# Optimization experiments

Hardware: AMD Instinct MI355X
Metric: run time of the kernel (lower is better)

## Reference

```python
import jax, jax.numpy as jnp
import numpy as np

T = 32768   # time points
N = 256     # state dim
NI = 32     # input dim
NO = 32     # output dim

# Dopri5 Butcher tableau (solution weights; b7 = 0 so only 6 stages needed)
_C = np.array([0.0, 1/5, 3/10, 4/5, 8/9, 1.0], dtype=np.float32)
_A21 = 1/5
_A31, _A32 = 3/40, 9/40
_A41, _A42, _A43 = 44/45, -56/15, 32/9
_A51, _A52, _A53, _A54 = 19372/6561, -25360/2187, 64448/6561, -212/729
_A61, _A62, _A63, _A64, _A65 = 9017/3168, -355/33, 46732/5247, 49/176, -5103/18656
_B1, _B3, _B4, _B5, _B6 = 35/384, 500/1113, 125/192, -2187/6784, 11/84

# Hermite cubic basis evaluated at the 6 stage offsets c in [0,1]: H[s, j]
s = _C
_H = np.stack([2*s**3 - 3*s**2 + 1,   # h00 * u_n
               s**3 - 2*s**2 + s,     # h10 * m_n (dt-scaled slope)
               -2*s**3 + 3*s**2,      # h01 * u_{n+1}
               s**3 - s**2], axis=1).astype(np.float32)  # h11 * m_{n+1}


def setup_inputs() -> dict:
    key = jax.random.key(0)
    k1, k2, k3, k4, k5, k6 = jax.random.split(key, 6)
    t = jnp.arange(T, dtype=jnp.float32)  # uniform grid, dt = 1
    u = jax.random.normal(k1, (T, NI), jnp.float32)
    x0 = jax.random.normal(k2, (N,), jnp.float32)
    # Stable linear system so fixed-step integration does not blow up
    A = jax.random.normal(k3, (N, N), jnp.float32) * (0.01 / np.sqrt(N)) - 0.02 * jnp.eye(N, dtype=jnp.float32)
    B = jax.random.normal(k4, (N, NI), jnp.float32) * (0.01 / np.sqrt(NI))
    C = jax.random.normal(k5, (NO, N), jnp.float32) / np.sqrt(N)
    D = jax.random.normal(k6, (NO, NI), jnp.float32) / np.sqrt(NI)
    return {"t": t, "u": u, "initial_state": x0, "A": A, "B": B, "C": C, "D": D}


def _stage_inputs(u):
    """Cubic-Hermite interpolation of u at the 6 Dopri5 stage times of each interval.
    Slopes via finite differences (dt-scaled, so index units suffice on a uniform grid).
    Returns [T-1, 6, NI]."""
    m = jnp.concatenate([u[1:2] - u[0:1],
                         (u[2:] - u[:-2]) * 0.5,
                         u[-1:] - u[-2:-1]], axis=0)
    P = jnp.stack([u[:-1], m[:-1], u[1:], m[1:]], axis=1)  # [T-1, 4, NI]
    return jnp.einsum('sj,tjd->tsd', jnp.asarray(_H), P)


def reference(t, u, initial_state, A, B, C, D):
    dt = t[1] - t[0]
    us = _stage_inputs(u)  # [T-1, 6, NI]

    def f(x, uu):  # vector field: dx/dt = A x + B u(t)
        return A @ x + B @ uu

    def step(x, us_n):
        k1 = f(x, us_n[0])
        k2 = f(x + dt * (_A21 * k1), us_n[1])
        k3 = f(x + dt * (_A31 * k1 + _A32 * k2), us_n[2])
        k4 = f(x + dt * (_A41 * k1 + _A42 * k2 + _A43 * k3), us_n[3])
        k5 = f(x + dt * (_A51 * k1 + _A52 * k2 + _A53 * k3 + _A54 * k4), us_n[4])
        k6 = f(x + dt * (_A61 * k1 + _A62 * k2 + _A63 * k3 + _A64 * k4 + _A65 * k5), us_n[5])
        x_new = x + dt * (_B1 * k1 + _B3 * k3 + _B4 * k4 + _B5 * k5 + _B6 * k6)
        return x_new, x_new

    _, xs = jax.lax.scan(step, initial_state, us)
    x = jnp.concatenate([initial_state[None], xs], axis=0)  # [T, N]
    y = x @ C.T + u @ D.T  # output: y = C x + D u, vmapped over time by broadcasting
    return (x, y)
```

## Files before the change

kernel.cpp:

```cpp
#include <hip/hip_runtime.h>


#define TPTS 32768

typedef __attribute__((ext_vector_type(8))) short short8;
typedef __attribute__((ext_vector_type(4))) float float4v;
typedef unsigned short ushort_t;

__device__ __forceinline__ ushort_t bf16_hi(float f) {
  unsigned u = __builtin_bit_cast(unsigned, f);
  unsigned r = (u + 0x7FFFu + ((u >> 16) & 1u)) >> 16;
  return (ushort_t)r;
}
__device__ __forceinline__ float bf16_f(ushort_t h) {
  unsigned u = ((unsigned)h) << 16;
  return __builtin_bit_cast(float, u);
}

template <int MODE, int CLEN>
__global__ __launch_bounds__(1024, 4) void chain_mfma(const ushort_t* Mh, const ushort_t* Ml,
                                                      const float* X0, const float* V,
                                                      float* Out, ushort_t* OutH, ushort_t* OutL) {
  constexpr int STEPS = (MODE == 0) ? CLEN : CLEN - 1;
  constexpr int HSLOTS = (MODE == 2) ? 5 : 1;
  int blk = blockIdx.x, t = threadIdx.x;
  int w = t >> 6, l = t & 63;
  int q = l >> 4, c16 = l & 15;
  int n0 = w * 16;
  short8 bh[8], bl[8];
#pragma unroll
  for (int kt = 0; kt < 8; kt++) {
    size_t offs = (size_t)(n0 + c16) * 256 + kt * 32 + q * 8;
    bh[kt] = *(const short8*)(Mh + offs);
    bl[kt] = *(const short8*)(Ml + offs);
  }
  __shared__ __attribute__((aligned(16))) ushort_t xh[2][32][16][8];
  __shared__ __attribute__((aligned(16))) ushort_t xl[2][32][16][8];
  __shared__ float hist[HSLOTS][16][256];
  {
    int e = t;
    int c = e >> 6, qq = (e & 63) * 4;
    int cg = blk * 16 + c;
    float4 v4;
    if (MODE == 0) {
      v4 = make_float4(qq == cg ? 1.f : 0.f, qq + 1 == cg ? 1.f : 0.f,
                       qq + 2 == cg ? 1.f : 0.f, qq + 3 == cg ? 1.f : 0.f);
    } else if (MODE == 1) {
      v4 = *(const float4*)(V + (size_t)cg * CLEN * 256 + qq);
    } else {
      v4 = *(const float4*)(X0 + (size_t)cg * 256 + qq);
      *(float4*)(Out + ((size_t)cg * CLEN) * 256 + qq) = v4;
    }
    float vals[4] = {v4.x, v4.y, v4.z, v4.w};
#pragma unroll
    for (int i = 0; i < 4; i++) {
      int n = qq + i;
      ushort_t h = bf16_hi(vals[i]);
      xh[0][n >> 3][c][n & 7] = h;
      xl[0][n >> 3][c][n & 7] = bf16_hi(vals[i] - bf16_f(h));
    }
  }
  float vnext[4];
  if (MODE != 0) {
#pragma unroll
    for (int r = 0; r < 4; r++) {
      int cg = blk * 16 + q * 4 + r;
      int drow = (MODE == 1) ? 1 : 0;
      vnext[r] = V[((size_t)cg * CLEN + drow) * 256 + n0 + c16];
    }
  }
  __syncthreads();
// ... 1 lines not shown
    int cur = (s - 1) & 1, nxt = s & 1;
    if (MODE == 2 && s >= 5 && ((s - 1) & 3) == 0) {
      int rbase = s - 4;
      for (int e = t; e < 4096; e += 1024) {
        int slot = e >> 10;
        int rem = e & 1023;
        int c = rem >> 6, qq = (rem & 63) * 4;
        int row = rbase + slot;
        int cg = blk * 16 + c;
        *(float4*)(Out + ((size_t)cg * CLEN + row) * 256 + qq) = *(const float4*)&hist[row % 5][c][qq];
      }
    }
    float vc[4];
    if (MODE != 0) {
#pragma unroll
      for (int i2 = 0; i2 < 4; i2++) vc[i2] = vnext[i2];
      if (s < STEPS) {
        int drow = (MODE == 1) ? (s + 1) : s;
#pragma unroll
        for (int r = 0; r < 4; r++)
          vnext[r] = V[((size_t)(blk * 16 + q * 4 + r) * CLEN + drow) * 256 + n0 + c16];
      }
    }
#pragma unroll
    for (int kt = 0; kt < 8; kt++) {
      asm volatile("" : "+v"(bh[kt]));
      asm volatile("" : "+v"(bl[kt]));
    }
    float4v aH = {0.f, 0.f, 0.f, 0.f};
    float4v aL = {0.f, 0.f, 0.f, 0.f};
    float4v aC = {0.f, 0.f, 0.f, 0.f};
#pragma unroll
    for (int kt = 0; kt < 8; kt++) {
      short8 ah = *(const short8*)&xh[cur][kt * 4 + q][c16][0];
      short8 al = *(const short8*)&xl[cur][kt * 4 + q][c16][0];
      aH = __builtin_amdgcn_mfma_f32_16x16x32_bf16(ah, bh[kt], aH, 0, 0, 0);
      aL = __builtin_amdgcn_mfma_f32_16x16x32_bf16(al, bh[kt], aL, 0, 0, 0);
      aC = __builtin_amdgcn_mfma_f32_16x16x32_bf16(ah, bl[kt], aC, 0, 0, 0);
    }
#pragma unroll
    for (int r = 0; r < 4; r++) {
      int c = q * 4 + r;
      int n = n0 + c16;
      float val = aH[r] + aL[r] + aC[r];
      if (MODE != 0) val += vc[r];
      int cg = blk * 16 + c;
      if (MODE == 2) hist[s % 5][c][n] = val;
      if (MODE == 1 && s == STEPS) Out[(size_t)cg * 256 + n] = val;
      if (MODE == 0 && s == STEPS) {
        ushort_t h2 = bf16_hi(val);
        Out[(size_t)n * 256 + cg] = val;
        OutH[(size_t)n * 256 + cg] = h2;
        OutL[(size_t)n * 256 + cg] = bf16_hi(val - bf16_f(h2));
      }
      ushort_t h = bf16_hi(val);
      xh[nxt][n >> 3][c][n & 7] = h;
      xl[nxt][n >> 3][c][n & 7] = bf16_hi(val - bf16_f(h));
    }
    __syncthreads();
  }
  if (MODE == 2) {
    for (int e = t; e < 3072; e += 1024) {
      int slot = e >> 10;
      int rem = e & 1023;
      int c = rem >> 6, qq = (rem & 63) * 4;
      int row = (STEPS - 2) + slot;
      int cg = blk * 16 + c;
      *(float4*)(Out + ((size_t)cg * CLEN + row) * 256 + qq) = *(const float4*)&hist[row % 5][c][qq];
    }
  }
}

__global__ __launch_bounds__(256) void gemm128(const float* __restrict__ A, const float* __restrict__ B,
                                               float* __restrict__ C, int M, int K) {
  int m0 = blockIdx.x * 128, n0 = blockIdx.y * 128;
  __shared__ float As[8][128];
  __shared__ float Bs[8][128];
  int tid = threadIdx.x;
  int am = tid >> 1, akc = (tid & 1) * 4;
  int bk = tid >> 5, bn = (tid & 31) * 4;
  int ty = tid >> 4, tx = tid & 15;
  float acc[8][8] = {{0.f}};
  for (int kt = 0; kt < K; kt += 8) {
    float4 av = make_float4(0.f, 0.f, 0.f, 0.f);
    if (m0 + am < M) av = *(const float4*)(A + (size_t)(m0 + am) * K + kt + akc);
    float4 bv = *(const float4*)(B + (size_t)(kt + bk) * 256 + n0 + bn);
    __syncthreads();
    As[akc + 0][am] = av.x;
    As[akc + 1][am] = av.y;
    As[akc + 2][am] = av.z;
    As[akc + 3][am] = av.w;
    *(float4*)&Bs[bk][bn] = bv;
    __syncthreads();
#pragma unroll
    for (int kk = 0; kk < 8; kk++) {
      float4 a0 = *(const float4*)&As[kk][ty * 8];
      float4 a1 = *(const float4*)&As[kk][ty * 8 + 4];
      float4 b0 = *(const float4*)&Bs[kk][tx * 8];
      float4 b1 = *(const float4*)&Bs[kk][tx * 8 + 4];
      float ar[8] = {a0.x, a0.y, a0.z, a0.w, a1.x, a1.y, a1.z, a1.w};
      float br[8] = {b0.x, b0.y, b0.z, b0.w, b1.x, b1.y, b1.z, b1.w};
#pragma unroll
      for (int i = 0; i < 8; i++)
#pragma unroll
        for (int j = 0; j < 8; j++) acc[i][j] += ar[i] * br[j];
    }
  }
#pragma unroll
  for (int i = 0; i < 8; i++) {
    int row = m0 + ty * 8 + i;
    if (row < M) {
      *(float4*)&C[(size_t)row * 256 + n0 + tx * 8] = make_float4(acc[i][0], acc[i][1], acc[i][2], acc[i][3]);
      *(float4*)&C[(size_t)row * 256 + n0 + tx * 8 + 4] = make_float4(acc[i][4], acc[i][5], acc[i][6], acc[i][7]);
    }
  }
}

__global__ __launch_bounds__(256) void transpose_at(const float* __restrict__ A, float* __restrict__ AT) {
  __shared__ float tile[64][65];
  int bx = blockIdx.x & 3, by = blockIdx.x >> 2;
  int r0 = by * 64, c0 = bx * 64;
  int t = threadIdx.x;
  int lr = t >> 4, lc = (t & 15) * 4;
  for (int rr = lr; rr < 64; rr += 16) {
    float4 v = *(const float4*)(A + (size_t)(r0 + rr) * 256 + c0 + lc);
    tile[rr][lc + 0] = v.x; tile[rr][lc + 1] = v.y; tile[rr][lc + 2] = v.z; tile[rr][lc + 3] = v.w;
  }
  __syncthreads();
  for (int rr = lr; rr < 64; rr += 16) {
    float4 v = make_float4(tile[lc + 0][rr], tile[lc + 1][rr], tile[lc + 2][rr], tile[lc + 3][rr]);
    *(float4*)(AT + (size_t)(c0 + rr) * 256 + r0 + lc) = v;
  }
}

__global__ __launch_bounds__(1024) void unit_resp(const float* __restrict__ AT,
                                                  const float* __restrict__ Bm,
                                                  float* __restrict__ Rout,
                                                  ushort_t* __restrict__ Rh,
                                                  ushort_t* __restrict__ Rl,
                                                  float* __restrict__ FcatT) {
  int blk = blockIdx.x;
  int tid = threadIdx.x;
  int jg = tid >> 8;
  int i = tid & 255;
  int cc = jg;
  int col = blk * 4 + cc;

  __shared__ float xs4[256][4];
  __shared__ float4 part[4][256];

  const float AA[6][5] = {
      {0.f, 0.f, 0.f, 0.f, 0.f},
      {0.2f, 0.f, 0.f, 0.f, 0.f},
      {3.f / 40.f, 9.f / 40.f, 0.f, 0.f, 0.f},
      {44.f / 45.f, -56.f / 15.f, 32.f / 9.f, 0.f, 0.f},
// ... 45 lines not shown
    float acx = 0.f, acy = 0.f, acz = 0.f, acw = 0.f;
#pragma unroll 8
    for (int jj = 0; jj < 64; jj++) {
      int j = j0 + jj;
      float a = AT[(size_t)j * 256 + i];
      float4 xv = *(const float4*)xs4[j];
      acx += a * xv.x;
      acy += a * xv.y;
      acz += a * xv.z;
      acw += a * xv.w;
    }
    part[jg][i] = make_float4(acx, acy, acz, acw);
    __syncthreads();
    float k = bh[s];
#pragma unroll
    for (int g = 0; g < 4; g++) {
      const float* p = (const float*)&part[g][i];
      k += p[cc];
    }
    kreg[s] = k;
  }

  float o = xc;
#pragma unroll
  for (int s = 0; s < 6; s++) o += BB[s] * kreg[s];
  if (!isF) {
    Rout[(size_t)i * 256 + col] = o;
    ushort_t h = bf16_hi(o);
    Rh[(size_t)i * 256 + col] = h;
    Rl[(size_t)i * 256 + col] = bf16_hi(o - bf16_f(h));
  } else {
    FcatT[(size_t)(col - 256) * 256 + i] = o;
  }
}

__global__ __launch_bounds__(128) void build_wtap(const float* __restrict__ u, float* __restrict__ Wtap) {
  int n = blockIdx.x;
  int tid = threadIdx.x;
  int t = tid >> 5, c = tid & 31;
  float val = 0.f;
  if (n < TPTS - 1) {
    if (t == 0) val = u[(size_t)n * 32 + c];
    else if (t == 2) val = u[(size_t)(n + 1) * 32 + c];
    else {
      int k = (t == 1) ? n : n + 1;
      if (k == 0) val = u[32 + c] - u[c];
      else if (k == TPTS - 1) val = u[(size_t)(TPTS - 1) * 32 + c] - u[(size_t)(TPTS - 2) * 32 + c];
      else val = 0.5f * (u[(size_t)(k + 1) * 32 + c] - u[(size_t)(k - 1) * 32 + c]);
    }
  }
  Wtap[(size_t)n * 128 + tid] = val;
}

__global__ __launch_bounds__(256) void top_scan(const float* __restrict__ V3, const float* __restrict__ x0,
                                                const float* __restrict__ R512, float* __restrict__ X3) {
  int k = blockIdx.x, i = threadIdx.x;
  if (k == 0) { X3[i] = x0[i]; return; }
  __shared__ float va[256];
  __shared__ float inner[256];
  if (k == 1) {
    inner[i] = x0[i];
  } else {
    const float* vecA = (k == 2) ? x0 : (V3 + (size_t)(k - 3) * 256);
    va[i] = vecA[i];
    __syncthreads();
    float acc = V3[(size_t)(k - 2) * 256 + i];
    const float* rr = R512 + (size_t)i * 256;
    for (int j = 0; j < 256; j += 4) {
      float4 rv = *(const float4*)(rr + j);
      acc += rv.x * va[j] + rv.y * va[j + 1] + rv.z * va[j + 2] + rv.w * va[j + 3];
    }
    inner[i] = acc;
  }
  __syncthreads();
  float acc2 = V3[(size_t)(k - 1) * 256 + i];
  const float* rr2 = R512 + (size_t)i * 256;
  for (int j = 0; j < 256; j += 4) {
    float4 rv = *(const float4*)(rr2 + j);
    acc2 += rv.x * inner[j] + rv.y * inner[j + 1] + rv.z * inner[j + 2] + rv.w * inner[j + 3];
  }
  X3[(size_t)k * 256 + i] = acc2;
}

__global__ __launch_bounds__(256) void y_kernel(const float* __restrict__ x, const float* __restrict__ u,
                                                const float* __restrict__ Cm, const float* __restrict__ Dm,
                                                float* __restrict__ y) {
  __shared__ float CsT[256][36];
  __shared__ float DsT[32][36];
  int tid = threadIdx.x;
  for (int k = tid; k < 8192; k += 256) CsT[k & 255][k >> 8] = Cm[k];
  for (int k = tid; k < 1024; k += 256) DsT[k & 31][k >> 5] = Dm[k];
  __syncthreads();
  int rt = tid >> 3, ct = tid & 7;
  int n0 = blockIdx.x * 128 + rt * 4;
  int o0 = ct * 4;
  float acc[4][4] = {{0.f}};
#pragma unroll 4
  for (int i = 0; i < 256; i += 4) {
    float4 cv0 = *(const float4*)&CsT[i + 0][o0];
    float4 cv1 = *(const float4*)&CsT[i + 1][o0];
    float4 cv2 = *(const float4*)&CsT[i + 2][o0];
    float4 cv3 = *(const float4*)&CsT[i + 3][o0];
#pragma unroll
    for (int r = 0; r < 4; r++) {
      float4 xv = *(const float4*)(x + (size_t)(n0 + r) * 256 + i);
      acc[r][0] += xv.x * cv0.x + xv.y * cv1.x + xv.z * cv2.x + xv.w * cv3.x;
      acc[r][1] += xv.x * cv0.y + xv.y * cv1.y + xv.z * cv2.y + xv.w * cv3.y;
      acc[r][2] += xv.x * cv0.z + xv.y * cv1.z + xv.z * cv2.z + xv.w * cv3.z;
      acc[r][3] += xv.x * cv0.w + xv.y * cv1.w + xv.z * cv2.w + xv.w * cv3.w;
    }
  }
#pragma unroll
  for (int i = 0; i < 32; i += 4) {
    float4 dv0 = *(const float4*)&DsT[i + 0][o0];
    float4 dv1 = *(const float4*)&DsT[i + 1][o0];
    float4 dv2 = *(const float4*)&DsT[i + 2][o0];
    float4 dv3 = *(const float4*)&DsT[i + 3][o0];
#pragma unroll
    for (int r = 0; r < 4; r++) {
      float4 uv = *(const float4*)(u + (size_t)(n0 + r) * 32 + i);
      acc[r][0] += uv.x * dv0.x + uv.y * dv1.x + uv.z * dv2.x + uv.w * dv3.x;
      acc[r][1] += uv.x * dv0.y + uv.y * dv1.y + uv.z * dv2.y + uv.w * dv3.y;
      acc[r][2] += uv.x * dv0.z + uv.y * dv1.z + uv.z * dv2.z + uv.w * dv3.z;
      acc[r][3] += uv.x * dv0.w + uv.y * dv1.w + uv.z * dv2.w + uv.w * dv3.w;
    }
  }
#pragma unroll
  for (int r = 0; r < 4; r++)
    *(float4*)(y + (size_t)(n0 + r) * 32 + o0) =
        make_float4(acc[r][0], acc[r][1], acc[r][2], acc[r][3]);
}

extern "C" void kernel_launch(void* const* d_in, const int* in_sizes, int n_in,
                              void* d_out, int out_size, void* d_ws, size_t ws_size,
                              hipStream_t stream) {
  const float* u  = (const float*)d_in[1];
  const float* x0 = (const float*)d_in[2];
  const float* A  = (const float*)d_in[3];
  const float* Bm = (const float*)d_in[4];
  const float* Cm = (const float*)d_in[5];
  const float* Dm = (const float*)d_in[6];
  float* xout = (float*)d_out;
  float* yout = xout + (size_t)TPTS * 256;

  char* wsb = (char*)d_ws;
  size_t off = 0;
  auto alloc = [&](size_t bytes) -> void* {
    void* p = (void*)(wsb + off);
    off = (off + bytes + 255) & ~(size_t)255;
    return p;
  };
  float*    Rfp    = (float*)alloc(65536 * 4);
  ushort_t* Rh     = (ushort_t*)alloc(65536 * 2);
  ushort_t* Rl     = (ushort_t*)alloc(65536 * 2);
  float*    PowFp  = (float*)alloc(65536 * 4);
  ushort_t* R8h    = (ushort_t*)alloc(65536 * 2);
  ushort_t* R8l    = (ushort_t*)alloc(65536 * 2);
  ushort_t* R64h   = (ushort_t*)alloc(65536 * 2);
  ushort_t* R64l   = (ushort_t*)alloc(65536 * 2);
  float*    R512fp = (float*)alloc(65536 * 4);
  ushort_t* R512h  = (ushort_t*)alloc(65536 * 2);
  ushort_t* R512l  = (ushort_t*)alloc(65536 * 2);
  float*    ATm    = (float*)alloc(65536 * 4);
  float*    FcatT  = (float*)alloc(128 * 256 * 4);
  float*    Wtap   = (float*)alloc((size_t)TPTS * 128 * 4);
  float*    V0     = (float*)alloc((size_t)TPTS * 256 * 4);
  float*    V1     = (float*)alloc(4096 * 256 * 4);
  float*    V2     = (float*)alloc(512 * 256 * 4);
  float*    V3     = (float*)alloc(64 * 256 * 4);
  float*    X3     = (float*)alloc(64 * 256 * 4);
  float*    X2     = (float*)alloc(512 * 256 * 4);
  float*    X1     = (float*)alloc(4096 * 256 * 4);
  (void)ws_size; (void)in_sizes; (void)n_in; (void)out_size;

  transpose_at<<<dim3(16), dim3(256), 0, stream>>>(A, ATm);
  unit_resp<<<dim3(96), dim3(1024), 0, stream>>>(ATm, Bm, Rfp, Rh, Rl, FcatT);

  chain_mfma<0, 8><<<dim3(16), dim3(1024), 0, stream>>>(Rh, Rl, nullptr, nullptr, PowFp, R8h, R8l);
  chain_mfma<0, 8><<<dim3(16), dim3(1024), 0, stream>>>(R8h, R8l, nullptr, nullptr, PowFp, R64h, R64l);
  chain_mfma<0, 8><<<dim3(16), dim3(1024), 0, stream>>>(R64h, R64l, nullptr, nullptr, R512fp, R512h, R512l);

  build_wtap<<<dim3(TPTS), dim3(128), 0, stream>>>(u, Wtap);
  gemm128<<<dim3(256, 2), dim3(256), 0, stream>>>(Wtap, FcatT, V0, TPTS, 128);

  chain_mfma<1, 8><<<dim3(256), dim3(1024), 0, stream>>>(Rh, Rl, nullptr, V0, V1, nullptr, nullptr);
  chain_mfma<1, 8><<<dim3(32), dim3(1024), 0, stream>>>(R8h, R8l, nullptr, V1, V2, nullptr, nullptr);
  chain_mfma<1, 8><<<dim3(4), dim3(1024), 0, stream>>>(R64h, R64l, nullptr, V2, V3, nullptr, nullptr);

  top_scan<<<dim3(64), dim3(256), 0, stream>>>(V3, x0, R512fp, X3);
  chain_mfma<2, 8><<<dim3(4), dim3(1024), 0, stream>>>(R64h, R64l, X3, V2, X2, nullptr, nullptr);
  chain_mfma<2, 8><<<dim3(32), dim3(1024), 0, stream>>>(R8h, R8l, X2, V1, X1, nullptr, nullptr);
  chain_mfma<2, 8><<<dim3(256), dim3(1024), 0, stream>>>(Rh, Rl, X1, V0, xout, nullptr, nullptr);

  y_kernel<<<dim3(256), dim3(256), 0, stream>>>(xout, u, Cm, Dm, yout);
}
```

Before: 342.3 us.

## Fuse scan chain into persistent megakernel with grid barriers and fused drive GEMM

Replaces about ten separate chain, top-scan and output kernel launches with one persistent 256-block kernel. The stages are separated by a software grid barrier built on atomics, and independent stages (power chains and the first-level scan) share phases. The Wtap build is folded into the GEMM's operand load, which removes a large intermediate buffer and one launch. The design relies on all 256 blocks of 1024 threads being co-resident, since the barrier would deadlock otherwise, and it adds barrier latency while many blocks sit idle in the small phases.

Result: slower. 1.111 ms (+224.5%).

```diff
diff --git a/kernel.cpp b/kernel.cpp
--- a/kernel.cpp
+++ b/kernel.cpp
@@ -17,16 +17,36 @@
   return __builtin_bit_cast(float, u);
 }
 
+__device__ __forceinline__ void grid_bar(unsigned* cnt, unsigned* gen) {
+  __syncthreads();
+  if (threadIdx.x == 0) {
+    __threadfence();
+    unsigned g = __hip_atomic_load(gen, __ATOMIC_RELAXED, __HIP_MEMORY_SCOPE_AGENT);
+    unsigned a = __hip_atomic_fetch_add(cnt, 1u, __ATOMIC_ACQ_REL, __HIP_MEMORY_SCOPE_AGENT);
+    if (a == 255u) {
+      __hip_atomic_store(cnt, 0u, __ATOMIC_RELAXED, __HIP_MEMORY_SCOPE_AGENT);
+      __hip_atomic_store(gen, g + 1u, __ATOMIC_RELEASE, __HIP_MEMORY_SCOPE_AGENT);
+    } else {
+      while (__hip_atomic_load(gen, __ATOMIC_ACQUIRE, __HIP_MEMORY_SCOPE_AGENT) == g)
+        __builtin_amdgcn_s_sleep(2);
+    }
+    __threadfence();
+  }
+  __syncthreads();
+}
+
 template <int MODE, int CLEN>
-__global__ __launch_bounds__(1024, 4) void chain_mfma(const ushort_t* Mh, const ushort_t* Ml,
-                                                      const float* X0, const float* V,
-                                                      float* Out, ushort_t* OutH, ushort_t* OutL) {
+__device__ __forceinline__ void chain_body(char* arena, const ushort_t* Mh, const ushort_t* Ml,
+                                           const float* X0, const float* V,
+                                           float* Out, ushort_t* OutH, ushort_t* OutL, int blk) {
   constexpr int STEPS = (MODE == 0) ? CLEN : CLEN - 1;
-  constexpr int HSLOTS = (MODE == 2) ? 5 : 1;
-  int blk = blockIdx.x, t = threadIdx.x;
+  int t = threadIdx.x;
   int w = t >> 6, l = t & 63;
   int q = l >> 4, c16 = l & 15;
   int n0 = w * 16;
+  ushort_t (*xh)[32][16][8] = reinterpret_cast<ushort_t(*)[32][16][8]>(arena);
+  ushort_t (*xl)[32][16][8] = reinterpret_cast<ushort_t(*)[32][16][8]>(arena + 16384);
+  float (*hist)[16][256] = reinterpret_cast<float(*)[16][256]>(arena + 32768);
   short8 bh[8], bl[8];
 #pragma unroll
   for (int kt = 0; kt < 8; kt++) {
@@ -34,9 +54,6 @@
     bh[kt] = *(const short8*)(Mh + offs);
     bl[kt] = *(const short8*)(Ml + offs);
   }
-  __shared__ __attribute__((aligned(16))) ushort_t xh[2][32][16][8];
-  __shared__ __attribute__((aligned(16))) ushort_t xl[2][32][16][8];
-  __shared__ float hist[HSLOTS][16][256];
   {
     int e = t;
     int c = e >> 6, qq = (e & 63) * 4;
@@ -104,11 +121,13 @@
     float4v aC = {0.f, 0.f, 0.f, 0.f};
 #pragma unroll
     for (int kt = 0; kt < 8; kt++) {
-      short8 ah = *(const short8*)&xh[cur][kt * 4 + q][c16][0];
-      short8 al = *(const short8*)&xl[cur][kt * 4 + q][c16][0];
-      aH = __builtin_amdgcn_mfma_f32_16x16x32_bf16(ah, bh[kt], aH, 0, 0, 0);
-      aL = __builtin_amdgcn_mfma_f32_16x16x32_bf16(al, bh[kt], aL, 0, 0, 0);
-      aC = __builtin_amdgcn_mfma_f32_16x16x32_bf16(ah, bl[kt], aC, 0, 0, 0);
+      short8 ah = *(const short8*)&(*xh)[0][0][0];
+      (void)ah;
+      short8 ah2 = *(const short8*)&xh[cur][kt * 4 + q][c16][0];
+      short8 al2 = *(const short8*)&xl[cur][kt * 4 + q][c16][0];
+      aH = __builtin_amdgcn_mfma_f32_16x16x32_bf16(ah2, bh[kt], aH, 0, 0, 0);
+      aL = __builtin_amdgcn_mfma_f32_16x16x32_bf16(al2, bh[kt], aL, 0, 0, 0);
+      aC = __builtin_amdgcn_mfma_f32_16x16x32_bf16(ah2, bl[kt], aC, 0, 0, 0);
     }
 #pragma unroll
     for (int r = 0; r < 4; r++) {
@@ -143,8 +162,148 @@
   }
 }
 
-__global__ __launch_bounds__(256) void gemm128(const float* __restrict__ A, const float* __restrict__ B,
-                                               float* __restrict__ C, int M, int K) {
+__global__ __launch_bounds__(1024, 4) void mega_scan(
+    const ushort_t* Rh, const ushort_t* Rl,
+    ushort_t* R8h, ushort_t* R8l, ushort_t* R64h, ushort_t* R64l,
+    float* R512fp, ushort_t* R512h, ushort_t* R512l, float* PowFp,
+    const float* V0, float* V1, float* V2, float* V3,
+    const float* x0, float* X3, float* X2, float* X1,
+    float* xout, const float* u, const float* Cm, const float* Dm, float* yout,
+    unsigned* bar) {
+  __shared__ __attribute__((aligned(16))) char arena[114688];
+  int blk = blockIdx.x;
+  int t = threadIdx.x;
+  unsigned* cnt = bar;
+  unsigned* gen = bar + 1;
+
+  if (blk < 16)
+    chain_body<0, 8>(arena, Rh, Rl, nullptr, nullptr, PowFp, R8h, R8l, blk);
+  else
+    chain_body<1, 8>(arena, Rh, Rl, nullptr, V0, V1, nullptr, nullptr, blk - 16);
+  grid_bar(cnt, gen);
+
+  if (blk < 16)
+    chain_body<1, 8>(arena, Rh, Rl, nullptr, V0, V1, nullptr, nullptr, 240 + blk);
+  else if (blk < 32)
+    chain_body<0, 8>(arena, R8h, R8l, nullptr, nullptr, PowFp, R64h, R64l, blk - 16);
+  grid_bar(cnt, gen);
+
+  if (blk < 32)
+    chain_body<1, 8>(arena, R8h, R8l, nullptr, V1, V2, nullptr, nullptr, blk);
+  else if (blk < 48)
+    chain_body<0, 8>(arena, R64h, R64l, nullptr, nullptr, R512fp, R512h, R512l, blk - 32);
+  grid_bar(cnt, gen);
+
+  if (blk < 4)
+    chain_body<1, 8>(arena, R64h, R64l, nullptr, V2, V3, nullptr, nullptr, blk);
+  grid_bar(cnt, gen);
+
+  {
+    float* va = ((float*)arena) + (t >> 8) * 256;
+    float* inner = ((float*)arena) + 1024 + (t >> 8) * 256;
+    int ug = t >> 8, i = t & 255;
+    int k = blk * 4 + ug;
+    bool act = (blk < 16);
+    if (act) {
+      if (k >= 3)      va[i] = V3[(size_t)(k - 3) * 256 + i];
+      else if (k == 2) va[i] = x0[i];
+      else             va[i] = 0.f;
+    }
+    __syncthreads();
+    if (act) {
+      float innv = 0.f;
+      if (k == 1) innv = x0[i];
+      else if (k >= 2) {
+        float acc = V3[(size_t)(k - 2) * 256 + i];
+        const float* rr = R512fp + (size_t)i * 256;
+        for (int j = 0; j < 256; j += 4) {
+          float4 rv = *(const float4*)(rr + j);
+          acc += rv.x * va[j] + rv.y * va[j + 1] + rv.z * va[j + 2] + rv.w * va[j + 3];
+        }
+        innv = acc;
+      }
+      inner[i] = innv;
+    }
+    __syncthreads();
+    if (act) {
+      if (k == 0) {
+        X3[i] = x0[i];
+      } else {
+        float acc2 = V3[(size_t)(k - 1) * 256 + i];
+        const float* rr2 = R512fp + (size_t)i * 256;
+        for (int j = 0; j < 256; j += 4) {
+          float4 rv = *(const float4*)(rr2 + j);
+          acc2 += rv.x * inner[j] + rv.y * inner[j + 1] + rv.z * inner[j + 2] + rv.w * inner[j + 3];
+        }
+        X3[(size_t)k * 256 + i] = acc2;
+      }
+    }
+  }
+  grid_bar(cnt, gen);
+
+  if (blk < 4)
+    chain_body<2, 8>(arena, R64h, R64l, X3, V2, X2, nullptr, nullptr, blk);
+  grid_bar(cnt, gen);
+
+  if (blk < 32)
+    chain_body<2, 8>(arena, R8h, R8l, X2, V1, X1, nullptr, nullptr, blk);
+  grid_bar(cnt, gen);
+
+  chain_body<2, 8>(arena, Rh, Rl, X1, V0, xout, nullptr, nullptr, blk);
+  grid_bar(cnt, gen);
+
+  {
+    float (*CsT)[36] = reinterpret_cast<float(*)[36]>(arena);
+    float (*DsT)[36] = reinterpret_cast<float(*)[36]>(arena + 36864);
+    for (int k2 = t; k2 < 8192; k2 += 1024) CsT[k2 & 255][k2 >> 8] = Cm[k2];
+    for (int k2 = t; k2 < 1024; k2 += 1024) DsT[k2 & 31][k2 >> 5] = Dm[k2];
+    __syncthreads();
+    if (t < 256) {
+      int rt = t >> 3, ct = t & 7;
+      int n0 = blk * 128 + rt * 4;
+      int o0 = ct * 4;
+      float acc[4][4] = {{0.f}};
+#pragma unroll 4
+      for (int i = 0; i < 256; i += 4) {
+        float4 cv0 = *(const float4*)&CsT[i + 0][o0];
+        float4 cv1 = *(const float4*)&CsT[i + 1][o0];
+        float4 cv2 = *(const float4*)&CsT[i + 2][o0];
+        float4 cv3 = *(const float4*)&CsT[i + 3][o0];
+#pragma unroll
+        for (int r = 0; r < 4; r++) {
+          float4 xv = *(const float4*)(xout + (size_t)(n0 + r) * 256 + i);
+          acc[r][0] += xv.x * cv0.x + xv.y * cv1.x + xv.z * cv2.x + xv.w * cv3.x;
+          acc[r][1] += xv.x * cv0.y + xv.y * cv1.y + xv.z * cv2.y + xv.w * cv3.y;
+          acc[r][2] += xv.x * cv0.z + xv.y * cv1.z + xv.z * cv2.z + xv.w * cv3.z;
+          acc[r][3] += xv.x * cv0.w + xv.y * cv1.w + xv.z * cv2.w + xv.w * cv3.w;
+        }
+      }
+#pragma unroll
+      for (int i = 0; i < 32; i += 4) {
+        float4 dv0 = *(const float4*)&DsT[i + 0][o0];
+        float4 dv1 = *(const float4*)&DsT[i + 1][o0];
+        float4 dv2 = *(const float4*)&DsT[i + 2][o0];
+        float4 dv3 = *(const float4*)&DsT[i + 3][o0];
+#pragma unroll
+        for (int r = 0; r < 4; r++) {
+          float4 uv = *(const float4*)(u + (size_t)(n0 + r) * 32 + i);
+          acc[r][0] += uv.x * dv0.x + uv.y * dv1.x + uv.z * dv2.x + uv.w * dv3.x;
+          acc[r][1] += uv.x * dv0.y + uv.y * dv1.y + uv.z * dv2.y + uv.w * dv3.y;
+          acc[r][2] += uv.x * dv0.z + uv.y * dv1.z + uv.z * dv2.z + uv.w * dv3.z;
+          acc[r][3] += uv.x * dv0.w + uv.y * dv1.w + uv.z * dv2.w + uv.w * dv3.w;
+        }
+      }
+#pragma unroll
+      for (int r = 0; r < 4; r++)
+        *(float4*)(yout + (size_t)(n0 + r) * 32 + o0) =
+            make_float4(acc[r][0], acc[r][1], acc[r][2], acc[r][3]);
+    }
+  }
+}
+
+__global__ __launch_bounds__(256) void gemm_drive(const float* __restrict__ u,
+                                                  const float* __restrict__ B,
+                                                  float* __restrict__ C, int M) {
   int m0 = blockIdx.x * 128, n0 = blockIdx.y * 128;
   __shared__ float As[8][128];
   __shared__ float Bs[8][128];
@@ -152,10 +311,41 @@
   int am = tid >> 1, akc = (tid & 1) * 4;
   int bk = tid >> 5, bn = (tid & 31) * 4;
   int ty = tid >> 4, tx = tid & 15;
+  int n = m0 + am;
   float acc[8][8] = {{0.f}};
-  for (int kt = 0; kt < K; kt += 8) {
+  for (int kt = 0; kt < 128; kt += 8) {
+    int tt = kt >> 5;
+    int cb = (kt & 31) + akc;
     float4 av = make_float4(0.f, 0.f, 0.f, 0.f);
-    if (m0 + am < M) av = *(const float4*)(A + (size_t)(m0 + am) * K + kt + akc);
+    if (n < TPTS - 1) {
+      if (tt == 0) {
+        av = *(const float4*)(u + (size_t)n * 32 + cb);
+      } else if (tt == 1) {
+        if (n == 0) {
+          float4 a1 = *(const float4*)(u + 32 + cb);
+          float4 a0 = *(const float4*)(u + cb);
+          av = make_float4(a1.x - a0.x, a1.y - a0.y, a1.z - a0.z, a1.w - a0.w);
+        } else {
+          float4 ap = *(const float4*)(u + (size_t)(n + 1) * 32 + cb);
+          float4 am4 = *(const float4*)(u + (size_t)(n - 1) * 32 + cb);
+          av = make_float4(0.5f * (ap.x - am4.x), 0.5f * (ap.y - am4.y),
+                           0.5f * (ap.z - am4.z), 0.5f * (ap.w - am4.w));
+        }
+      } else if (tt == 2) {
+        av = *(const float4*)(u + (size_t)(n + 1) * 32 + cb);
+      } else {
+        if (n + 1 == TPTS - 1) {
+          float4 a1 = *(const float4*)(u + (size_t)(TPTS - 1) * 32 + cb);
+          float4 a0 = *(const float4*)(u + (size_t)(TPTS - 2) * 32 + cb);
+          av = make_float4(a1.x - a0.x, a1.y - a0.y, a1.z - a0.z, a1.w - a0.w);
+        } else {
+          float4 ap = *(const float4*)(u + (size_t)(n + 2) * 32 + cb);
+          float4 am4 = *(const float4*)(u + (size_t)n * 32 + cb);
+          av = make_float4(0.5f * (ap.x - am4.x), 0.5f * (ap.y - am4.y),
+                           0.5f * (ap.z - am4.z), 0.5f * (ap.w - am4.w));
+        }
+      }
+    }
     float4 bv = *(const float4*)(B + (size_t)(kt + bk) * 256 + n0 + bn);
     __syncthreads();
     As[akc + 0][am] = av.x;
@@ -188,11 +378,13 @@
   }
 }
 
-__global__ __launch_bounds__(256) void transpose_at(const float* __restrict__ A, float* __restrict__ AT) {
+__global__ __launch_bounds__(256) void transpose_at(const float* __restrict__ A, float* __restrict__ AT,
+                                                    unsigned* bar) {
   __shared__ float tile[64][65];
   int bx = blockIdx.x & 3, by = blockIdx.x >> 2;
   int r0 = by * 64, c0 = bx * 64;
   int t = threadIdx.x;
+  if (blockIdx.x == 0 && t == 0) { bar[0] = 0u; bar[1] = 0u; }
   int lr = t >> 4, lc = (t & 15) * 4;
   for (int rr = lr; rr < 64; rr += 16) {
     float4 v = *(const float4*)(A + (size_t)(r0 + rr) * 256 + c0 + lc);
@@ -304,103 +496,6 @@
   } else {
     FcatT[(size_t)(col - 256) * 256 + i] = o;
   }
-}
-
-__global__ __launch_bounds__(128) void build_wtap(const float* __restrict__ u, float* __restrict__ Wtap) {
-  int n = blockIdx.x;
-  int tid = threadIdx.x;
-  int t = tid >> 5, c = tid & 31;
-  float val = 0.f;
-  if (n < TPTS - 1) {
-    if (t == 0) val = u[(size_t)n * 32 + c];
-    else if (t == 2) val = u[(size_t)(n + 1) * 32 + c];
-    else {
-      int k = (t == 1) ? n : n + 1;
-      if (k == 0) val = u[32 + c] - u[c];
-      else if (k == TPTS - 1) val = u[(size_t)(TPTS - 1) * 32 + c] - u[(size_t)(TPTS - 2) * 32 + c];
-      else val = 0.5f * (u[(size_t)(k + 1) * 32 + c] - u[(size_t)(k - 1) * 32 + c]);
-    }
-  }
-  Wtap[(size_t)n * 128 + tid] = val;
-}
-
-__global__ __launch_bounds__(256) void top_scan(const float* __restrict__ V3, const float* __restrict__ x0,
-                                                const float* __restrict__ R512, float* __restrict__ X3) {
-  int k = blockIdx.x, i = threadIdx.x;
-  if (k == 0) { X3[i] = x0[i]; return; }
-  __shared__ float va[256];
-  __shared__ float inner[256];
-  if (k == 1) {
-    inner[i] = x0[i];
-  } else {
-    const float* vecA = (k == 2) ? x0 : (V3 + (size_t)(k - 3) * 256);
-    va[i] = vecA[i];
-    __syncthreads();
-    float acc = V3[(size_t)(k - 2) * 256 + i];
-    const float* rr = R512 + (size_t)i * 256;
-    for (int j = 0; j < 256; j += 4) {
-      float4 rv = *(const float4*)(rr + j);
-      acc += rv.x * va[j] + rv.y * va[j + 1] + rv.z * va[j + 2] + rv.w * va[j + 3];
-    }
-    inner[i] = acc;
-  }
-  __syncthreads();
-  float acc2 = V3[(size_t)(k - 1) * 256 + i];
-  const float* rr2 = R512 + (size_t)i * 256;
-  for (int j = 0; j < 256; j += 4) {
-    float4 rv = *(const float4*)(rr2 + j);
-    acc2 += rv.x * inner[j] + rv.y * inner[j + 1] + rv.z * inner[j + 2] + rv.w * inner[j + 3];
-  }
-  X3[(size_t)k * 256 + i] = acc2;
-}
-
-__global__ __launch_bounds__(256) void y_kernel(const float* __restrict__ x, const float* __restrict__ u,
-                                                const float* __restrict__ Cm, const float* __restrict__ Dm,
-                                                float* __restrict__ y) {
-  __shared__ float CsT[256][36];
-  __shared__ float DsT[32][36];
-  int tid = threadIdx.x;
-  for (int k = tid; k < 8192; k += 256) CsT[k & 255][k >> 8] = Cm[k];
-  for (int k = tid; k < 1024; k += 256) DsT[k & 31][k >> 5] = Dm[k];
-  __syncthreads();
-  int rt = tid >> 3, ct = tid & 7;
-  int n0 = blockIdx.x * 128 + rt * 4;
-  int o0 = ct * 4;
-  float acc[4][4] = {{0.f}};
-#pragma unroll 4
-  for (int i = 0; i < 256; i += 4) {
-    float4 cv0 = *(const float4*)&CsT[i + 0][o0];
-    float4 cv1 = *(const float4*)&CsT[i + 1][o0];
-    float4 cv2 = *(const float4*)&CsT[i + 2][o0];
-    float4 cv3 = *(const float4*)&CsT[i + 3][o0];
-#pragma unroll
-    for (int r = 0; r < 4; r++) {
-      float4 xv = *(const float4*)(x + (size_t)(n0 + r) * 256 + i);
-      acc[r][0] += xv.x * cv0.x + xv.y * cv1.x + xv.z * cv2.x + xv.w * cv3.x;
-      acc[r][1] += xv.x * cv0.y + xv.y * cv1.y + xv.z * cv2.y + xv.w * cv3.y;
-      acc[r][2] += xv.x * cv0.z + xv.y * cv1.z + xv.z * cv2.z + xv.w * cv3.z;
-      acc[r][3] += xv.x * cv0.w + xv.y * cv1.w + xv.z * cv2.w + xv.w * cv3.w;
-    }
-  }
-#pragma unroll
-  for (int i = 0; i < 32; i += 4) {
-    float4 dv0 = *(const float4*)&DsT[i + 0][o0];
-    float4 dv1 = *(const float4*)&DsT[i + 1][o0];
-    float4 dv2 = *(const float4*)&DsT[i + 2][o0];
-    float4 dv3 = *(const float4*)&DsT[i + 3][o0];
-#pragma unroll
-    for (int r = 0; r < 4; r++) {
-      float4 uv = *(const float4*)(u + (size_t)(n0 + r) * 32 + i);
-      acc[r][0] += uv.x * dv0.x + uv.y * dv1.x + uv.z * dv2.x + uv.w * dv3.x;
-      acc[r][1] += uv.x * dv0.y + uv.y * dv1.y + uv.z * dv2.y + uv.w * dv3.y;
-      acc[r][2] += uv.x * dv0.z + uv.y * dv1.z + uv.z * dv2.z + uv.w * dv3.z;
-      acc[r][3] += uv.x * dv0.w + uv.y * dv1.w + uv.z * dv2.w + uv.w * dv3.w;
-    }
-  }
-#pragma unroll
-  for (int r = 0; r < 4; r++)
-    *(float4*)(y + (size_t)(n0 + r) * 32 + o0) =
-        make_float4(acc[r][0], acc[r][1], acc[r][2], acc[r][3]);
 }
 
 extern "C" void kernel_launch(void* const* d_in, const int* in_sizes, int n_in,
@@ -435,7 +530,6 @@
   ushort_t* R512l  = (ushort_t*)alloc(65536 * 2);
   float*    ATm    = (float*)alloc(65536 * 4);
   float*    FcatT  = (float*)alloc(128 * 256 * 4);
-  float*    Wtap   = (float*)alloc((size_t)TPTS * 128 * 4);
   float*    V0     = (float*)alloc((size_t)TPTS * 256 * 4);
   float*    V1     = (float*)alloc(4096 * 256 * 4);
   float*    V2     = (float*)alloc(512 * 256 * 4);
@@ -443,26 +537,15 @@
   float*    X3     = (float*)alloc(64 * 256 * 4);
   float*    X2     = (float*)alloc(512 * 256 * 4);
   float*    X1     = (float*)alloc(4096 * 256 * 4);
+  unsigned* bar    = (unsigned*)alloc(256);
   (void)ws_size; (void)in_sizes; (void)n_in; (void)out_size;
 
-  transpose_at<<<dim3(16), dim3(256), 0, stream>>>(A, ATm);
+  transpose_at<<<dim3(16), dim3(256), 0, stream>>>(A, ATm, bar);
   unit_resp<<<dim3(96), dim3(1024), 0, stream>>>(ATm, Bm, Rfp, Rh, Rl, FcatT);
 
-  chain_mfma<0, 8><<<dim3(16), dim3(1024), 0, stream>>>(Rh, Rl, nullptr, nullptr, PowFp, R8h, R8l);
-  chain_mfma<0, 8><<<dim3(16), dim3(1024), 0, stream>>>(R8h, R8l, nullptr, nullptr, PowFp, R64h, R64l);
-  chain_mfma<0, 8><<<dim3(16), dim3(1024), 0, stream>>>(R64h, R64l, nullptr, nullptr, R512fp, R512h, R512l);
-
-  build_wtap<<<dim3(TPTS), dim3(128), 0, stream>>>(u, Wtap);
-  gemm128<<<dim3(256, 2), dim3(256), 0, stream>>>(Wtap, FcatT, V0, TPTS, 128);
-
-  chain_mfma<1, 8><<<dim3(256), dim3(1024), 0, stream>>>(Rh, Rl, nullptr, V0, V1, nullptr, nullptr);
-  chain_mfma<1, 8><<<dim3(32), dim3(1024), 0, stream>>>(R8h, R8l, nullptr, V1, V2, nullptr, nullptr);
-  chain_mfma<1, 8><<<dim3(4), dim3(1024), 0, stream>>>(R64h, R64l, nullptr, V2, V3, nullptr, nullptr);
-
-  top_scan<<<dim3(64), dim3(256), 0, stream>>>(V3, x0, R512fp, X3);
-  chain_mfma<2, 8><<<dim3(4), dim3(1024), 0, stream>>>(R64h, R64l, X3, V2, X2, nullptr, nullptr);
-  chain_mfma<2, 8><<<dim3(32), dim3(1024), 0, stream>>>(R8h, R8l, X2, V1, X1, nullptr, nullptr);
-  chain_mfma<2, 8><<<dim3(256), dim3(1024), 0, stream>>>(Rh, Rl, X1, V0, xout, nullptr, nullptr);
-
-  y_kernel<<<dim3(256), dim3(256), 0, stream>>>(xout, u, Cm, Dm, yout);
-}
+  gemm_drive<<<dim3(256, 2), dim3(256), 0, stream>>>(u, FcatT, V0, TPTS);
+
+  mega_scan<<<dim3(256), dim3(1024), 0, stream>>>(
+      Rh, Rl, R8h, R8l, R64h, R64l, R512fp, R512h, R512l, PowFp,
+      V0, V1, V2, V3, x0, X3, X2, X1, xout, u, Cm, Dm, yout, bar);
+}
```

## Merge independent chain and GEMM kernels into shared launches, fuse tap build and y output

Applied to the files above, without the earlier changes.

Independent stages now share a launch through a block-index split: the matrix-power squarings run alongside the input GEMM and the reduction chains, so far fewer kernels are launched. The Wtap buffer is gone because the GEMM computes the Hermite tap values straight from u while loading tiles. The y = Cx + Du output is computed at the end of the final expansion kernel, reading back the freshly written x. The aim is to cut launch overhead and the Wtap round trip through memory. In exchange the GEMM moves to 1024-thread blocks with 4x4 tiles and scalar loads, and the expand kernels reserve a larger shared arena, which may lower occupancy.

Result: slower. 438.3 us (+28.1%).

```diff
diff --git a/kernel.cpp b/kernel.cpp
--- a/kernel.cpp
+++ b/kernel.cpp
@@ -18,15 +18,17 @@
 }
 
 template <int MODE, int CLEN>
-__global__ __launch_bounds__(1024, 4) void chain_mfma(const ushort_t* Mh, const ushort_t* Ml,
-                                                      const float* X0, const float* V,
-                                                      float* Out, ushort_t* OutH, ushort_t* OutL) {
+__device__ __forceinline__ void chain_body(char* arena, const ushort_t* Mh, const ushort_t* Ml,
+                                           const float* X0, const float* V,
+                                           float* Out, ushort_t* OutH, ushort_t* OutL, int blk) {
   constexpr int STEPS = (MODE == 0) ? CLEN : CLEN - 1;
-  constexpr int HSLOTS = (MODE == 2) ? 5 : 1;
-  int blk = blockIdx.x, t = threadIdx.x;
+  int t = threadIdx.x;
   int w = t >> 6, l = t & 63;
   int q = l >> 4, c16 = l & 15;
   int n0 = w * 16;
+  ushort_t (*xh)[32][16][8] = reinterpret_cast<ushort_t(*)[32][16][8]>(arena);
+  ushort_t (*xl)[32][16][8] = reinterpret_cast<ushort_t(*)[32][16][8]>(arena + 16384);
+  float (*hist)[16][256] = reinterpret_cast<float(*)[16][256]>(arena + 32768);
   short8 bh[8], bl[8];
 #pragma unroll
   for (int kt = 0; kt < 8; kt++) {
@@ -34,9 +36,6 @@
     bh[kt] = *(const short8*)(Mh + offs);
     bl[kt] = *(const short8*)(Ml + offs);
   }
-  __shared__ __attribute__((aligned(16))) ushort_t xh[2][32][16][8];
-  __shared__ __attribute__((aligned(16))) ushort_t xl[2][32][16][8];
-  __shared__ float hist[HSLOTS][16][256];
   {
     int e = t;
     int c = e >> 6, qq = (e & 63) * 4;
@@ -143,48 +142,161 @@
   }
 }
 
-__global__ __launch_bounds__(256) void gemm128(const float* __restrict__ A, const float* __restrict__ B,
-                                               float* __restrict__ C, int M, int K) {
-  int m0 = blockIdx.x * 128, n0 = blockIdx.y * 128;
-  __shared__ float As[8][128];
-  __shared__ float Bs[8][128];
+__device__ __forceinline__ float tap_val(const float* __restrict__ u, int n, int k) {
+  if (n >= TPTS - 1) return 0.f;
+  int t = k >> 5, c = k & 31;
+  if (t == 0) return u[(size_t)n * 32 + c];
+  if (t == 2) return u[(size_t)(n + 1) * 32 + c];
+  int kk = (t == 1) ? n : n + 1;
+  if (kk == 0) return u[32 + c] - u[c];
+  if (kk == TPTS - 1) return u[(size_t)(TPTS - 1) * 32 + c] - u[(size_t)(TPTS - 2) * 32 + c];
+  return 0.5f * (u[(size_t)(kk + 1) * 32 + c] - u[(size_t)(kk - 1) * 32 + c]);
+}
+
+__device__ __forceinline__ void gemm_body(char* arena, const float* __restrict__ u,
+                                          const float* __restrict__ B, float* __restrict__ C, int g) {
+  float (*As)[132] = reinterpret_cast<float(*)[132]>(arena);
+  float (*Bs)[128] = reinterpret_cast<float(*)[128]>(arena + 4224);
+  int m0 = (g & 255) * 128, n0 = (g >> 8) * 128;
   int tid = threadIdx.x;
-  int am = tid >> 1, akc = (tid & 1) * 4;
-  int bk = tid >> 5, bn = (tid & 31) * 4;
-  int ty = tid >> 4, tx = tid & 15;
-  float acc[8][8] = {{0.f}};
-  for (int kt = 0; kt < K; kt += 8) {
-    float4 av = make_float4(0.f, 0.f, 0.f, 0.f);
-    if (m0 + am < M) av = *(const float4*)(A + (size_t)(m0 + am) * K + kt + akc);
-    float4 bv = *(const float4*)(B + (size_t)(kt + bk) * 256 + n0 + bn);
+  int am = tid >> 3, ak = tid & 7;
+  int bk = tid >> 7, bn = tid & 127;
+  int ty = tid >> 5, tx = tid & 31;
+  float acc[4][4] = {{0.f}};
+  for (int kt = 0; kt < 128; kt += 8) {
+    float av = tap_val(u, m0 + am, kt + ak);
+    float bv = B[(size_t)(kt + bk) * 256 + n0 + bn];
     __syncthreads();
-    As[akc + 0][am] = av.x;
-    As[akc + 1][am] = av.y;
-    As[akc + 2][am] = av.z;
-    As[akc + 3][am] = av.w;
-    *(float4*)&Bs[bk][bn] = bv;
+    As[ak][am] = av;
+    Bs[bk][bn] = bv;
     __syncthreads();
 #pragma unroll
     for (int kk = 0; kk < 8; kk++) {
-      float4 a0 = *(const float4*)&As[kk][ty * 8];
-      float4 a1 = *(const float4*)&As[kk][ty * 8 + 4];
-      float4 b0 = *(const float4*)&Bs[kk][tx * 8];
-      float4 b1 = *(const float4*)&Bs[kk][tx * 8 + 4];
-      float ar[8] = {a0.x, a0.y, a0.z, a0.w, a1.x, a1.y, a1.z, a1.w};
-      float br[8] = {b0.x, b0.y, b0.z, b0.w, b1.x, b1.y, b1.z, b1.w};
-#pragma unroll
-      for (int i = 0; i < 8; i++)
-#pragma unroll
-        for (int j = 0; j < 8; j++) acc[i][j] += ar[i] * br[j];
-    }
-  }
-#pragma unroll
-  for (int i = 0; i < 8; i++) {
-    int row = m0 + ty * 8 + i;
-    if (row < M) {
-      *(float4*)&C[(size_t)row * 256 + n0 + tx * 8] = make_float4(acc[i][0], acc[i][1], acc[i][2], acc[i][3]);
-      *(float4*)&C[(size_t)row * 256 + n0 + tx * 8 + 4] = make_float4(acc[i][4], acc[i][5], acc[i][6], acc[i][7]);
-    }
+      float4 a = *(const float4*)&As[kk][ty * 4];
+      float4 b = *(const float4*)&Bs[kk][tx * 4];
+      float ar[4] = {a.x, a.y, a.z, a.w};
+      float br[4] = {b.x, b.y, b.z, b.w};
+#pragma unroll
+      for (int i = 0; i < 4; i++)
+#pragma unroll
+        for (int j = 0; j < 4; j++) acc[i][j] += ar[i] * br[j];
+    }
+  }
+#pragma unroll
+  for (int i = 0; i < 4; i++) {
+    int row = m0 + ty * 4 + i;
+    *(float4*)&C[(size_t)row * 256 + n0 + tx * 4] =
+        make_float4(acc[i][0], acc[i][1], acc[i][2], acc[i][3]);
+  }
+}
+
+__global__ __launch_bounds__(1024, 4) void pow8_gemm(const ushort_t* Rh, const ushort_t* Rl,
+                                                     float* PowFp, ushort_t* R8h, ushort_t* R8l,
+                                                     const float* u, const float* FcatT, float* V0) {
+  __shared__ __attribute__((aligned(16))) char arena[49152];
+  int blk = blockIdx.x;
+  if (blk < 16)
+    chain_body<0, 8>(arena, Rh, Rl, nullptr, nullptr, PowFp, R8h, R8l, blk);
+  else
+    gemm_body(arena, u, FcatT, V0, blk - 16);
+}
+
+__global__ __launch_bounds__(1024, 4) void pow64_reduce0(const ushort_t* R8h, const ushort_t* R8l,
+                                                         float* PowFp, ushort_t* R64h, ushort_t* R64l,
+                                                         const ushort_t* Rh, const ushort_t* Rl,
+                                                         const float* V0, float* V1) {
+  __shared__ __attribute__((aligned(16))) char arena[49152];
+  int blk = blockIdx.x;
+  if (blk < 16)
+    chain_body<0, 8>(arena, R8h, R8l, nullptr, nullptr, PowFp, R64h, R64l, blk);
+  else
+    chain_body<1, 8>(arena, Rh, Rl, nullptr, V0, V1, nullptr, nullptr, blk - 16);
+}
+
+__global__ __launch_bounds__(1024, 4) void pow512_reduce1(const ushort_t* R64h, const ushort_t* R64l,
+                                                          float* R512fp, ushort_t* R512h, ushort_t* R512l,
+                                                          const ushort_t* R8h, const ushort_t* R8l,
+                                                          const float* V1, float* V2) {
+  __shared__ __attribute__((aligned(16))) char arena[49152];
+  int blk = blockIdx.x;
+  if (blk < 16)
+    chain_body<0, 8>(arena, R64h, R64l, nullptr, nullptr, R512fp, R512h, R512l, blk);
+  else
+    chain_body<1, 8>(arena, R8h, R8l, nullptr, V1, V2, nullptr, nullptr, blk - 16);
+}
+
+__global__ __launch_bounds__(1024, 4) void reduce2_k(const ushort_t* R64h, const ushort_t* R64l,
+                                                     const float* V2, float* V3) {
+  __shared__ __attribute__((aligned(16))) char arena[49152];
+  chain_body<1, 8>(arena, R64h, R64l, nullptr, V2, V3, nullptr, nullptr, blockIdx.x);
+}
+
+__global__ __launch_bounds__(1024, 4) void expand2_k(const ushort_t* R64h, const ushort_t* R64l,
+                                                     const float* X3, const float* V2, float* X2) {
+  __shared__ __attribute__((aligned(16))) char arena[114688];
+  chain_body<2, 8>(arena, R64h, R64l, X3, V2, X2, nullptr, nullptr, blockIdx.x);
+}
+
+__global__ __launch_bounds__(1024, 4) void expand1_k(const ushort_t* R8h, const ushort_t* R8l,
+                                                     const float* X2, const float* V1, float* X1) {
+  __shared__ __attribute__((aligned(16))) char arena[114688];
+  chain_body<2, 8>(arena, R8h, R8l, X2, V1, X1, nullptr, nullptr, blockIdx.x);
+}
+
+__global__ __launch_bounds__(1024, 4) void expand0_y(const ushort_t* Rh, const ushort_t* Rl,
+                                                     const float* X1, const float* V0, float* xout,
+                                                     const float* u, const float* Cm, const float* Dm,
+                                                     float* yout) {
+  __shared__ __attribute__((aligned(16))) char arena[114688];
+  int blk = blockIdx.x;
+  int t = threadIdx.x;
+  chain_body<2, 8>(arena, Rh, Rl, X1, V0, xout, nullptr, nullptr, blk);
+  __threadfence();
+  __syncthreads();
+  float (*CsT)[36] = reinterpret_cast<float(*)[36]>(arena);
+  float (*DsT)[36] = reinterpret_cast<float(*)[36]>(arena + 36864);
+  for (int k2 = t; k2 < 8192; k2 += 1024) CsT[k2 & 255][k2 >> 8] = Cm[k2];
+  for (int k2 = t; k2 < 1024; k2 += 1024) DsT[k2 & 31][k2 >> 5] = Dm[k2];
+  __syncthreads();
+  if (t < 256) {
+    int rt = t >> 3, ct = t & 7;
+    int n0 = blk * 128 + rt * 4;
+    int o0 = ct * 4;
+    float acc[4][4] = {{0.f}};
+#pragma unroll 4
+    for (int i = 0; i < 256; i += 4) {
+      float4 cv0 = *(const float4*)&CsT[i + 0][o0];
+      float4 cv1 = *(const float4*)&CsT[i + 1][o0];
+      float4 cv2 = *(const float4*)&CsT[i + 2][o0];
+      float4 cv3 = *(const float4*)&CsT[i + 3][o0];
+#pragma unroll
+      for (int r = 0; r < 4; r++) {
+        float4 xv = *(const float4*)(xout + (size_t)(n0 + r) * 256 + i);
+        acc[r][0] += xv.x * cv0.x + xv.y * cv1.x + xv.z * cv2.x + xv.w * cv3.x;
+        acc[r][1] += xv.x * cv0.y + xv.y * cv1.y + xv.z * cv2.y + xv.w * cv3.y;
+        acc[r][2] += xv.x * cv0.z + xv.y * cv1.z + xv.z * cv2.z + xv.w * cv3.z;
+        acc[r][3] += xv.x * cv0.w + xv.y * cv1.w + xv.z * cv2.w + xv.w * cv3.w;
+      }
+    }
+#pragma unroll
+    for (int i = 0; i < 32; i += 4) {
+      float4 dv0 = *(const float4*)&DsT[i + 0][o0];
+      float4 dv1 = *(const float4*)&DsT[i + 1][o0];
+      float4 dv2 = *(const float4*)&DsT[i + 2][o0];
+      float4 dv3 = *(const float4*)&DsT[i + 3][o0];
+#pragma unroll
+      for (int r = 0; r < 4; r++) {
+        float4 uv = *(const float4*)(u + (size_t)(n0 + r) * 32 + i);
+        acc[r][0] += uv.x * dv0.x + uv.y * dv1.x + uv.z * dv2.x + uv.w * dv3.x;
+        acc[r][1] += uv.x * dv0.y + uv.y * dv1.y + uv.z * dv2.y + uv.w * dv3.y;
+        acc[r][2] += uv.x * dv0.z + uv.y * dv1.z + uv.z * dv2.z + uv.w * dv3.z;
+        acc[r][3] += uv.x * dv0.w + uv.y * dv1.w + uv.z * dv2.w + uv.w * dv3.w;
+      }
+    }
+#pragma unroll
+    for (int r = 0; r < 4; r++)
+      *(float4*)(yout + (size_t)(n0 + r) * 32 + o0) =
+          make_float4(acc[r][0], acc[r][1], acc[r][2], acc[r][3]);
   }
 }
 
@@ -304,24 +416,6 @@
   } else {
     FcatT[(size_t)(col - 256) * 256 + i] = o;
   }
-}
-
-__global__ __launch_bounds__(128) void build_wtap(const float* __restrict__ u, float* __restrict__ Wtap) {
-  int n = blockIdx.x;
-  int tid = threadIdx.x;
-  int t = tid >> 5, c = tid & 31;
-  float val = 0.f;
-  if (n < TPTS - 1) {
-    if (t == 0) val = u[(size_t)n * 32 + c];
-    else if (t == 2) val = u[(size_t)(n + 1) * 32 + c];
-    else {
-      int k = (t == 1) ? n : n + 1;
-      if (k == 0) val = u[32 + c] - u[c];
-      else if (k == TPTS - 1) val = u[(size_t)(TPTS - 1) * 32 + c] - u[(size_t)(TPTS - 2) * 32 + c];
-      else val = 0.5f * (u[(size_t)(k + 1) * 32 + c] - u[(size_t)(k - 1) * 32 + c]);
-    }
-  }
-  Wtap[(size_t)n * 128 + tid] = val;
 }
 
 __global__ __launch_bounds__(256) void top_scan(const float* __restrict__ V3, const float* __restrict__ x0,
@@ -352,55 +446,6 @@
     acc2 += rv.x * inner[j] + rv.y * inner[j + 1] + rv.z * inner[j + 2] + rv.w * inner[j + 3];
   }
   X3[(size_t)k * 256 + i] = acc2;
-}
-
-__global__ __launch_bounds__(256) void y_kernel(const float* __restrict__ x, const float* __restrict__ u,
-                                                const float* __restrict__ Cm, const float* __restrict__ Dm,
-                                                float* __restrict__ y) {
-  __shared__ float CsT[256][36];
-  __shared__ float DsT[32][36];
-  int tid = threadIdx.x;
-  for (int k = tid; k < 8192; k += 256) CsT[k & 255][k >> 8] = Cm[k];
-  for (int k = tid; k < 1024; k += 256) DsT[k & 31][k >> 5] = Dm[k];
-  __syncthreads();
-  int rt = tid >> 3, ct = tid & 7;
-  int n0 = blockIdx.x * 128 + rt * 4;
-  int o0 = ct * 4;
-  float acc[4][4] = {{0.f}};
-#pragma unroll 4
-  for (int i = 0; i < 256; i += 4) {
-    float4 cv0 = *(const float4*)&CsT[i + 0][o0];
-    float4 cv1 = *(const float4*)&CsT[i + 1][o0];
-    float4 cv2 = *(const float4*)&CsT[i + 2][o0];
-    float4 cv3 = *(const float4*)&CsT[i + 3][o0];
-#pragma unroll
-    for (int r = 0; r < 4; r++) {
-      float4 xv = *(const float4*)(x + (size_t)(n0 + r) * 256 + i);
-      acc[r][0] += xv.x * cv0.x + xv.y * cv1.x + xv.z * cv2.x + xv.w * cv3.x;
-      acc[r][1] += xv.x * cv0.y + xv.y * cv1.y + xv.z * cv2.y + xv.w * cv3.y;
-      acc[r][2] += xv.x * cv0.z + xv.y * cv1.z + xv.z * cv2.z + xv.w * cv3.z;
-      acc[r][3] += xv.x * cv0.w + xv.y * cv1.w + xv.z * cv2.w + xv.w * cv3.w;
-    }
-  }
-#pragma unroll
-  for (int i = 0; i < 32; i += 4) {
-    float4 dv0 = *(const float4*)&DsT[i + 0][o0];
-    float4 dv1 = *(const float4*)&DsT[i + 1][o0];
-    float4 dv2 = *(const float4*)&DsT[i + 2][o0];
-    float4 dv3 = *(const float4*)&DsT[i + 3][o0];
-#pragma unroll
-    for (int r = 0; r < 4; r++) {
-      float4 uv = *(const float4*)(u + (size_t)(n0 + r) * 32 + i);
-      acc[r][0] += uv.x * dv0.x + uv.y * dv1.x + uv.z * dv2.x + uv.w * dv3.x;
-      acc[r][1] += uv.x * dv0.y + uv.y * dv1.y + uv.z * dv2.y + uv.w * dv3.y;
-      acc[r][2] += uv.x * dv0.z + uv.y * dv1.z + uv.z * dv2.z + uv.w * dv3.z;
-      acc[r][3] += uv.x * dv0.w + uv.y * dv1.w + uv.z * dv2.w + uv.w * dv3.w;
-    }
-  }
-#pragma unroll
-  for (int r = 0; r < 4; r++)
-    *(float4*)(y + (size_t)(n0 + r) * 32 + o0) =
-        make_float4(acc[r][0], acc[r][1], acc[r][2], acc[r][3]);
 }
 
 extern "C" void kernel_launch(void* const* d_in, const int* in_sizes, int n_in,
@@ -435,7 +480,6 @@
   ushort_t* R512l  = (ushort_t*)alloc(65536 * 2);
   float*    ATm    = (float*)alloc(65536 * 4);
   float*    FcatT  = (float*)alloc(128 * 256 * 4);
-  float*    Wtap   = (float*)alloc((size_t)TPTS * 128 * 4);
   float*    V0     = (float*)alloc((size_t)TPTS * 256 * 4);
   float*    V1     = (float*)alloc(4096 * 256 * 4);
   float*    V2     = (float*)alloc(512 * 256 * 4);
@@ -448,21 +492,16 @@
   transpose_at<<<dim3(16), dim3(256), 0, stream>>>(A, ATm);
   unit_resp<<<dim3(96), dim3(1024), 0, stream>>>(ATm, Bm, Rfp, Rh, Rl, FcatT);
 
-  chain_mfma<0, 8><<<dim3(16), dim3(1024), 0, stream>>>(Rh, Rl, nullptr, nullptr, PowFp, R8h, R8l);
-  chain_mfma<0, 8><<<dim3(16), dim3(1024), 0, stream>>>(R8h, R8l, nullptr, nullptr, PowFp, R64h, R64l);
-  chain_mfma<0, 8><<<dim3(16), dim3(1024), 0, stream>>>(R64h, R64l, nullptr, nullptr, R512fp, R512h, R512l);
-
-  build_wtap<<<dim3(TPTS), dim3(128), 0, stream>>>(u, Wtap);
-  gemm128<<<dim3(256, 2), dim3(256), 0, stream>>>(Wtap, FcatT, V0, TPTS, 128);
-
-  chain_mfma<1, 8><<<dim3(256), dim3(1024), 0, stream>>>(Rh, Rl, nullptr, V0, V1, nullptr, nullptr);
-  chain_mfma<1, 8><<<dim3(32), dim3(1024), 0, stream>>>(R8h, R8l, nullptr, V1, V2, nullptr, nullptr);
-  chain_mfma<1, 8><<<dim3(4), dim3(1024), 0, stream>>>(R64h, R64l, nullptr, V2, V3, nullptr, nullptr);
-
+  pow8_gemm<<<dim3(528), dim3(1024), 0, stream>>>(Rh, Rl, PowFp, R8h, R8l, u, FcatT, V0);
+
+  pow64_reduce0<<<dim3(272), dim3(1024), 0, stream>>>(R8h, R8l, PowFp, R64h, R64l, Rh, Rl, V0, V1);
+
+  pow512_reduce1<<<dim3(48), dim3(1024), 0, stream>>>(R64h, R64l, R512fp, R512h, R512l, R8h, R8l, V1, V2);
+
+  reduce2_k<<<dim3(4), dim3(1024), 0, stream>>>(R64h, R64l, V2, V3);
   top_scan<<<dim3(64), dim3(256), 0, stream>>>(V3, x0, R512fp, X3);
-  chain_mfma<2, 8><<<dim3(4), dim3(1024), 0, stream>>>(R64h, R64l, X3, V2, X2, nullptr, nullptr);
-  chain_mfma<2, 8><<<dim3(32), dim3(1024), 0, stream>>>(R8h, R8l, X2, V1, X1, nullptr, nullptr);
-  chain_mfma<2, 8><<<dim3(256), dim3(1024), 0, stream>>>(Rh, Rl, X1, V0, xout, nullptr, nullptr);
-
-  y_kernel<<<dim3(256), dim3(256), 0, stream>>>(xout, u, Cm, Dm, yout);
-}
+  expand2_k<<<dim3(4), dim3(1024), 0, stream>>>(R64h, R64l, X3, V2, X2);
+  expand1_k<<<dim3(32), dim3(1024), 0, stream>>>(R8h, R8l, X2, V1, X1);
+
+  expand0_y<<<dim3(256), dim3(1024), 0, stream>>>(Rh, Rl, X1, V0, xout, u, Cm, Dm, yout);
+}
```
